# Kernel optimization log

Measured on AMD Instinct MI355X. Metric: run time of the kernel, lower is better.

## Reference

```python
import jax, jax.numpy as jnp
import numpy as np

B_, S_, D_ = 2, 1024, 768
EXPAND, HEADDIM, DSTATE = 2, 64, 64
DINNER = EXPAND * D_            # 1536
NHEADS = DINNER // HEADDIM      # 24
DMLP = int(2.5 * D_)            # 1920
PROJ = 2 * DINNER + 2 * NHEADS * DSTATE + NHEADS + NHEADS * (DSTATE // 2)  # 6936


def rms_norm(x, w, eps=1e-5):
    return x * jax.lax.rsqrt(jnp.mean(x * x, axis=-1, keepdims=True) + eps) * w


def apply_rope(x, angles):
    # x: (..., d_state), angles: (..., d_state//2)
    x1 = x[..., 0::2]
    x2 = x[..., 1::2]
    c, s = jnp.cos(angles), jnp.sin(angles)
    even = c * x1 - s * x2
    odd = s * x1 + c * x2
    return jnp.stack([even, odd], axis=-1).reshape(x.shape)


def ssm_scan(x, A, Bm, Cm):
    # x: (b,s,h,p), A: (b,s,h), Bm/Cm: (b,s,h,n)
    b, s, h, p = x.shape
    n = Bm.shape[-1]

    def step(hstate, inp):
        x_t, A_t, B_t, C_t = inp
        hstate = hstate * jnp.exp(A_t)[:, :, None, None] + jnp.einsum('bhn,bhp->bhpn', B_t, x_t)
        y_t = jnp.einsum('bhpn,bhn->bhp', hstate, C_t)
        return hstate, y_t

    h0 = jnp.zeros((b, h, p, n), dtype=x.dtype)
    xs = (jnp.swapaxes(x, 0, 1), jnp.swapaxes(A, 0, 1),
          jnp.swapaxes(Bm, 0, 1), jnp.swapaxes(Cm, 0, 1))
    _, ys = jax.lax.scan(step, h0, xs)
    return jnp.swapaxes(ys, 0, 1)  # (b,s,h,p)


def setup_inputs() -> dict:
    key = jax.random.key(0)
    ks = jax.random.split(key, 16)
    sc = 0.02
    return {
        'x': jax.random.normal(ks[0], (B_, S_, D_), dtype=jnp.float32),
        'norm1_w': jnp.ones((D_,), jnp.float32),
        'norm2_w': jnp.ones((D_,), jnp.float32),
        'in_proj_w': jax.random.normal(ks[1], (PROJ, D_), jnp.float32) * sc,
        'out_proj_w': jax.random.normal(ks[2], (D_, DINNER), jnp.float32) * sc,
        'A_log': jax.random.uniform(ks[3], (NHEADS,), jnp.float32, -4.0, -1.0),
        'D': jnp.ones((NHEADS,), jnp.float32),
        'dt_bias': jax.random.uniform(ks[4], (NHEADS,), jnp.float32, 0.001, 0.1),
        'B_bias': jnp.ones((1, NHEADS, DSTATE), jnp.float32),
        'C_bias': jnp.ones((1, NHEADS, DSTATE), jnp.float32),
        'Bnorm_w': jnp.ones((DSTATE,), jnp.float32),
        'Cnorm_w': jnp.ones((DSTATE,), jnp.float32),
        'mlp_gate_w': jax.random.normal(ks[5], (DMLP, D_), jnp.float32) * sc,
        'mlp_up_w': jax.random.normal(ks[6], (DMLP, D_), jnp.float32) * sc,
        'mlp_down_w': jax.random.normal(ks[7], (D_, DMLP), jnp.float32) * sc,
    }


def reference(x, norm1_w, norm2_w, in_proj_w, out_proj_w, A_log, D, dt_bias,
              B_bias, C_bias, Bnorm_w, Cnorm_w, mlp_gate_w, mlp_up_w, mlp_down_w):
    b, s, _ = x.shape
    h = rms_norm(x, norm1_w)
    proj = jnp.einsum('bsd,od->bso', h, in_proj_w)
    i = 0
    z = proj[..., i:i + DINNER]; i += DINNER
    x_ssm = proj[..., i:i + DINNER]; i += DINNER
    Bm = proj[..., i:i + NHEADS * DSTATE].reshape(b, s, NHEADS, DSTATE); i += NHEADS * DSTATE
    Cm = proj[..., i:i + NHEADS * DSTATE].reshape(b, s, NHEADS, DSTATE); i += NHEADS * DSTATE
    dt = proj[..., i:i + NHEADS]; i += NHEADS
    theta = proj[..., i:].reshape(b, s, NHEADS, DSTATE // 2)

    dt = jax.nn.softplus(dt + dt_bias)                 # (b,s,h)
    A = -jnp.exp(A_log) * dt                           # (b,s,h)
    alpha = jnp.exp(A)
    gamma = (alpha - 1.0) / (A + 1e-6) * 0.5 + 1.0

    Bm = rms_norm(Bm, Bnorm_w) + B_bias
    Cm = rms_norm(Cm, Cnorm_w) + C_bias
    cum_theta = jnp.cumsum(dt[..., None] * theta, axis=1)
    Bm = apply_rope(Bm, cum_theta)
    Cm = apply_rope(Cm, cum_theta)

    x_ssm = x_ssm.reshape(b, s, NHEADS, HEADDIM)
    x_scaled = x_ssm * gamma[..., None]
    y = ssm_scan(x_scaled, A, Bm, Cm)                  # (b,s,h,p)
    skip = (D[None, None, :] * x_ssm.sum(-1))[..., None]  # (b,s,h,1)
    y = (y + skip).reshape(b, s, DINNER)
    y = y * (z * jax.nn.sigmoid(z))
    y = jnp.einsum('bsi,oi->bso', y, out_proj_w)
    x = x + y
    h2 = rms_norm(x, norm2_w)
    g = jnp.einsum('bsd,od->bso', h2, mlp_gate_w)
    u = jnp.einsum('bsd,od->bso', h2, mlp_up_w)
    mlp = jnp.einsum('bsi,oi->bso', (g * jax.nn.sigmoid(g)) * u, mlp_down_w)
    return x + mlp
```

## Files before the change

kernel.cpp:

```cpp
#include <hip/hip_runtime.h>

typedef unsigned short u16;
typedef __attribute__((ext_vector_type(8))) short short8;
typedef __attribute__((ext_vector_type(4))) float f32x4;

constexpr int B_N    = 2;
constexpr int SEQ    = 1024;
constexpr int DMODEL = 768;
constexpr int DINNER = 1536;
constexpr int NH     = 24;
constexpr int DMLP   = 1920;
constexpr int NPROJ  = 6936;
constexpr int PP     = 7040;
constexpr int MROWS  = B_N * SEQ;
constexpr int NCHUNK = 16;
constexpr int CLEN   = 64;

__device__ __forceinline__ u16 f2bf(float f) {
  union { float f; unsigned u; } x; x.f = f;
  unsigned r = x.u + 0x7fffu + ((x.u >> 16) & 1u);
  return (u16)(r >> 16);
}
__device__ __forceinline__ float bf2f(u16 b) {
  union { unsigned u; float f; } x; x.u = ((unsigned)b) << 16; return x.f;
}

__device__ __forceinline__ void gld_lds16(const u16* g, u16* l) {
  __builtin_amdgcn_global_load_lds((const __attribute__((address_space(1))) void*)g,
                                   (__attribute__((address_space(3))) void*)l, 16, 0, 0);
}

__device__ __forceinline__ short8 frag(const u16* base, int row, int cb) {
  return *(const short8*)(base + row * 64 + ((cb ^ (row & 7)) << 3));
}
__device__ __forceinline__ int swz_idx(int row, int e) {
  return (((e >> 3) ^ (row & 7)) << 3) | (e & 7);
}

constexpr size_t E0  = (size_t)PP * DMODEL;
constexpr size_t E0s = (size_t)NPROJ * DMODEL;
constexpr size_t E1  = (size_t)DMODEL * DINNER;
constexpr size_t E2  = (size_t)DMLP * DMODEL;
constexpr size_t ETOT = E0 + E1 + 3 * E2;

__global__ void cast_all_kernel(const float* __restrict__ w_in, const float* __restrict__ w_out,
                                const float* __restrict__ w_g, const float* __restrict__ w_u,
                                const float* __restrict__ w_d,
                                u16* __restrict__ wb_in, u16* __restrict__ wb_out,
                                u16* __restrict__ wb_gu, u16* __restrict__ wb_d) {
  size_t i = ((size_t)blockIdx.x * 256 + threadIdx.x) * 4;
  if (i >= ETOT) return;
  float4 v; u16* dst;
  if (i < E0) {
    dst = wb_in + i;
    if (i < E0s) v = *(const float4*)(w_in + i);
    else { v.x = v.y = v.z = v.w = 0.f; }
  } else if (i < E0 + E1) {
    size_t k = i - E0; dst = wb_out + k; v = *(const float4*)(w_out + k);
  } else if (i < E0 + E1 + 2 * E2) {
    size_t k = i - E0 - E1;
    size_t r = k / DMODEL, col = k - r * DMODEL;
    const float* src = (r & 1) ? w_u : w_g;
    v = *(const float4*)(src + (r >> 1) * DMODEL + col);
    dst = wb_gu + k;
  } else {
    size_t k = i - E0 - E1 - 2 * E2; dst = wb_d + k; v = *(const float4*)(w_d + k);
  }
  short4 o;
  o.x = (short)f2bf(v.x); o.y = (short)f2bf(v.y);
  o.z = (short)f2bf(v.z); o.w = (short)f2bf(v.w);
  *(short4*)dst = o;
}

__global__ __launch_bounds__(256) void add_rmsnorm_kernel(
    const float* __restrict__ a, const float* __restrict__ b,
    const float* __restrict__ w, float* __restrict__ sum_out,
    u16* __restrict__ hout) {
  int row = blockIdx.x;
  int t = threadIdx.x;
  const float* pa = a + (size_t)row * DMODEL;
  const float* pb = b ? b + (size_t)row * DMODEL : nullptr;
  float v[3]; float ss = 0.f;
#pragma unroll
  for (int i = 0; i < 3; ++i) {
    int c = t + i * 256;
    float x = pa[c];
    if (pb) x += pb[c];
    v[i] = x; ss += x * x;
  }
#pragma unroll
  for (int o = 32; o > 0; o >>= 1) ss += __shfl_xor(ss, o);
  __shared__ float red[4];
  if ((t & 63) == 0) red[t >> 6] = ss;
  __syncthreads();
  ss = red[0] + red[1] + red[2] + red[3];
  float sc = rsqrtf(ss * (1.f / DMODEL) + 1e-5f);
#pragma unroll
  for (int i = 0; i < 3; ++i) {
    int c = t + i * 256;
    if (sum_out) sum_out[(size_t)row * DMODEL + c] = v[i];
    hout[(size_t)row * DMODEL + c] = f2bf(v[i] * sc * w[c]);
  }
}

template<int BM, int BN, int MODE>
__global__ __launch_bounds__(256) void gemm_bt_kernel(
    const u16* __restrict__ A, const u16* __restrict__ Bw,
    void* __restrict__ Cv, int K, int ldc, const float* __restrict__ addsrc) {
  constexpr int MI = BM / 32;
  constexpr int NJ = BN / 32;
  __shared__ u16 As[BM * 64];
  __shared__ u16 Bs[BN * 64];
  const int t = threadIdx.x;
  const int lane = t & 63;
  const int wave = t >> 6;
  const int wm = wave >> 1, wn = wave & 1;
  const int gx = gridDim.x, gy = gridDim.y;
  const int o = blockIdx.y * gx + blockIdx.x;
  const int nwg = gx * gy;
  const int cid = (o & 7) * (nwg >> 3) + (o >> 3);
  const int bx = cid / gy, by = cid - bx * gy;
  const int m0 = by * BM, n0 = bx * BN;
  f32x4 acc[MI][NJ] = {};
  const int rr = t >> 3;
  const int kc = (((t & 7) ^ (rr & 7))) * 8;
  const u16* ga = A + (size_t)(m0 + rr) * K + kc;
  const u16* gb = Bw + (size_t)(n0 + rr) * K + kc;
  for (int kt = 0; kt < K; kt += 64) {
    __syncthreads();
#pragma unroll
    for (int i = 0; i < MI; ++i)
      gld_lds16(ga + (size_t)i * 32 * K + kt, As + i * 2048 + t * 8);
#pragma unroll
    for (int i = 0; i < NJ; ++i)
      gld_lds16(gb + (size_t)i * 32 * K + kt, Bs + i * 2048 + t * 8);
    __syncthreads();
#pragma unroll
    for (int kh = 0; kh < 2; ++kh) {
      const int cq = kh * 4 + (lane >> 4);
      short8 af[MI], bfr[NJ];
#pragma unroll
      for (int i = 0; i < MI; ++i)
        af[i] = frag(As, wm * (BM / 2) + i * 16 + (lane & 15), cq);
#pragma unroll
      for (int j = 0; j < NJ; ++j)
        bfr[j] = frag(Bs, wn * (BN / 2) + j * 16 + (lane & 15), cq);
#pragma unroll
      for (int i = 0; i < MI; ++i)
#pragma unroll
        for (int j = 0; j < NJ; ++j)
          acc[i][j] = __builtin_amdgcn_mfma_f32_16x16x32_bf16(af[i], bfr[j], acc[i][j], 0, 0, 0);
    }
  }
  const int cr = (lane >> 4) * 4;
  const int cc = lane & 15;
#pragma unroll
  for (int i = 0; i < MI; ++i) {
#pragma unroll
    for (int j = 0; j < NJ; ++j) {
      int row = m0 + wm * (BM / 2) + i * 16 + cr;
      int col = n0 + wn * (BN / 2) + j * 16 + cc;
      if (MODE == 0) {
        float* C = (float*)Cv;
        float* cp = C + (size_t)row * ldc + col;
        if (addsrc) {
          const float* ap = addsrc + (size_t)row * ldc + col;
#pragma unroll
          for (int r = 0; r < 4; ++r) cp[(size_t)r * ldc] = acc[i][j][r] + ap[(size_t)r * ldc];
        } else {
#pragma unroll
          for (int r = 0; r < 4; ++r) cp[(size_t)r * ldc] = acc[i][j][r];
        }
      } else if (MODE == 1) {
        u16* C = (u16*)Cv;
#pragma unroll
        for (int r = 0; r < 4; ++r)
          C[(size_t)(row + r) * ldc + col] = f2bf(acc[i][j][r]);
      } else {
        u16* C = (u16*)Cv;
#pragma unroll
        for (int r = 0; r < 4; ++r) {
          float v = acc[i][j][r];
          float p = __shfl_xor(v, 1);
          if ((lane & 1) == 0) {
            float g = v, u = p;
            float res = g / (1.f + __expf(-g)) * u;
            C[(size_t)(row + r) * ldc + (col >> 1)] = f2bf(res);
          }
        }
      }
    }
  }
}

__global__ __launch_bounds__(256) void prep_kernel(
    u16* __restrict__ proj, const float* __restrict__ A_log,
    const float* __restrict__ Dv, const float* __restrict__ dt_bias,
    const float* __restrict__ B_bias, const float* __restrict__ C_bias,
    const float* __restrict__ Bnw, const float* __restrict__ Cnw,
    float* __restrict__ Abuf, float* __restrict__ skip_b,
    float* __restrict__ dtheta) {
  int wid = blockIdx.x * 4 + (threadIdx.x >> 6);
  int lane = threadIdx.x & 63;
  int m = wid / NH, h = wid - m * NH;
  u16* row = proj + (size_t)m * PP;

  float Braw = bf2f(row[3072 + h * 64 + lane]);
  float Craw = bf2f(row[4608 + h * 64 + lane]);
  float sb = Braw * Braw, sc2 = Craw * Craw;
#pragma unroll
  for (int o = 32; o > 0; o >>= 1) { sb += __shfl_xor(sb, o); sc2 += __shfl_xor(sc2, o); }
  float rb = rsqrtf(sb * (1.f / 64.f) + 1e-5f);
  float rc = rsqrtf(sc2 * (1.f / 64.f) + 1e-5f);
  row[3072 + h * 64 + lane] = f2bf(Braw * rb * Bnw[lane] + B_bias[h * 64 + lane]);
  row[4608 + h * 64 + lane] = f2bf(Craw * rc * Cnw[lane] + C_bias[h * 64 + lane]);

  float dtr = bf2f(row[6144 + h]) + dt_bias[h];
  float dt = dtr > 20.f ? dtr : log1pf(__expf(dtr));
  float A = -__expf(A_log[h]) * dt;
  float alpha = __expf(A);
  float gamma = (alpha - 1.f) / (A + 1e-6f) * 0.5f + 1.f;

  float xv = bf2f(row[1536 + h * 64 + lane]);
  float sx = xv;
#pragma unroll
  for (int o = 32; o > 0; o >>= 1) sx += __shfl_xor(sx, o);
  row[1536 + h * 64 + lane] = f2bf(xv * gamma);

  if (lane == 0) {
    Abuf[(size_t)m * NH + h] = A;
    skip_b[(size_t)m * NH + h] = Dv[h] * sx;
  }
  if (lane < 32) {
    float th = bf2f(row[6168 + h * 32 + lane]);
    dtheta[(size_t)m * 768 + h * 32 + lane] = dt * th;
  }
}

__global__ __launch_bounds__(256) void cumsum_a_kernel(float* __restrict__ dtheta,
                                                       float* __restrict__ ctot) {
  int bid = blockIdx.x;
  int cb = bid % 3, rest = bid / 3;
  int c = rest & 15, b = rest >> 4;
  int col = cb * 256 + threadIdx.x;
  float* p = dtheta + ((size_t)(b * SEQ + c * CLEN)) * 768 + col;
  float acc = 0.f;
#pragma unroll 4
  for (int s = 0; s < CLEN; ++s) {
    acc += p[(size_t)s * 768];
    p[(size_t)s * 768] = acc;
  }
  ctot[((size_t)b * NCHUNK + c) * 768 + col] = acc;
}

__global__ void cumsum_b_kernel(float* __restrict__ ctot) {
  int tid = blockIdx.x * 256 + threadIdx.x;
  int b = tid / 768, col = tid - b * 768;
  float pre = 0.f;
#pragma unroll
  for (int c = 0; c < NCHUNK; ++c) {
    size_t o = ((size_t)b * NCHUNK + c) * 768 + col;
    float v = ctot[o];
    ctot[o] = pre;
    pre += v;
  }
}

__global__ __launch_bounds__(256) void rope_kernel(
    u16* __restrict__ proj, const float* __restrict__ dtheta,
    const float* __restrict__ ctot) {
  int wid = blockIdx.x * 4 + (threadIdx.x >> 6);
  int lane = threadIdx.x & 63;
  int m = wid / NH, h = wid - m * NH;
  int j = lane & 31;
  int b = m >> 10;
  int c = (m >> 6) & 15;
  float ang = dtheta[(size_t)m * 768 + h * 32 + j] +
              ctot[((size_t)b * NCHUNK + c) * 768 + h * 32 + j];
  float sn, cs;
  __sincosf(ang, &sn, &cs);
  int base = (lane < 32) ? 3072 : 4608;
  unsigned* p = (unsigned*)(proj + (size_t)m * PP + base + h * 64) + j;
  unsigned v = *p;
  float x1 = bf2f((u16)(v & 0xffffu));
  float x2 = bf2f((u16)(v >> 16));
  *p = (unsigned)f2bf(cs * x1 - sn * x2) | ((unsigned)f2bf(sn * x1 + cs * x2) << 16);
}

__global__ __launch_bounds__(256) void scanA_kernel(
    const u16* __restrict__ proj, const float* __restrict__ Abuf,
    float* __restrict__ Lbuf, float* __restrict__ Hbuf,
    float* __restrict__ y1b) {
  int c = blockIdx.x & 15, bh = blockIdx.x >> 4;
  int b = bh / NH, h = bh - b * NH;
  int t = threadIdx.x, w = t >> 6, l = t & 63;
  __shared__ float sTmp[64][65];
  __shared__ u16 sBT[64 * 64];
  __shared__ u16 sXT[64 * 64];
  __shared__ u16 sGm[64 * 64];
  __shared__ float sRatio[64], sL[64];
  int m0 = b * SEQ + c * CLEN;
  if (w == 0) {
    float v = Abuf[(size_t)(m0 + l) * NH + h];
#pragma unroll
    for (int o = 1; o < 64; o <<= 1) {
      float u = __shfl_up(v, o);
      if (l >= o) v += u;
    }
    Lbuf[(size_t)(m0 + l) * NH + h] = v;
    sL[l] = v;
    float L63 = __shfl(v, 63);
    sRatio[l] = __expf(L63 - v);
  }
  int rr = t >> 2, q = t & 3;
  {
    const u16* row = proj + (size_t)(m0 + rr) * PP + 3072 + h * 64;
#pragma unroll
    for (int k = 0; k < 4; ++k) {
      int e = q * 16 + k * 4;
      short4 sv = *(const short4*)(row + e);
      float4 ov;
      ov.x = bf2f((u16)sv.x); ov.y = bf2f((u16)sv.y);
      ov.z = bf2f((u16)sv.z); ov.w = bf2f((u16)sv.w);
      *(float4*)&sTmp[rr][e] = ov;
    }
  }
  const u16* baseC = proj + (size_t)m0 * PP + 4608 + h * 64;
  const u16* baseB = proj + (size_t)m0 * PP + 3072 + h * 64;
  short8 cf[2], bgf[2][4];
#pragma unroll
  for (int kh = 0; kh < 2; ++kh) {
    int cq = kh * 4 + (l >> 4);
    cf[kh] = *(const short8*)(baseC + (size_t)(w * 16 + (l & 15)) * PP + cq * 8);
#pragma unroll
    for (int j = 0; j < 4; ++j)
      bgf[kh][j] = *(const short8*)(baseB + (size_t)(j * 16 + (l & 15)) * PP + cq * 8);
  }
  __syncthreads();
  f32x4 g4[4] = {};
#pragma unroll
  for (int kh = 0; kh < 2; ++kh)
#pragma unroll
    for (int j = 0; j < 4; ++j)
      g4[j] = __builtin_amdgcn_mfma_f32_16x16x32_bf16(cf[kh], bgf[kh][j], g4[j], 0, 0, 0);
  {
#pragma unroll
    for (int k = 0; k < 8; ++k) {
      int tw = (l + w * 8 + k) & 31;
      int t0 = tw * 2;
      float v0 = sTmp[t0][l] * sRatio[t0];
      float v1 = sTmp[t0 + 1][l] * sRatio[t0 + 1];
      unsigned pk = (unsigned)f2bf(v0) | ((unsigned)f2bf(v1) << 16);
      *(unsigned*)(sBT + l * 64 + swz_idx(l, t0)) = pk;
    }
  }
  __syncthreads();
  {
    const u16* row = proj + (size_t)(m0 + rr) * PP + 1536 + h * 64;
#pragma unroll
    for (int k = 0; k < 4; ++k) {
      int e = q * 16 + k * 4;
      short4 sv = *(const short4*)(row + e);
      float4 ov;
      ov.x = bf2f((u16)sv.x); ov.y = bf2f((u16)sv.y);
      ov.z = bf2f((u16)sv.z); ov.w = bf2f((u16)sv.w);
      *(float4*)&sTmp[rr][e] = ov;
    }
  }
  __syncthreads();
  {
#pragma unroll
    for (int k = 0; k < 8; ++k) {
      int tw = (l + w * 8 + k) & 31;
      int t0 = tw * 2;
      unsigned pk = (unsigned)f2bf(sTmp[t0][l]) | ((unsigned)f2bf(sTmp[t0 + 1][l]) << 16);
      *(unsigned*)(sXT + l * 64 + swz_idx(l, t0)) = pk;
    }
  }
  {
    int sr = w * 16 + ((l >> 4) << 2);
#pragma unroll
    for (int j = 0; j < 4; ++j) {
      int tc = j * 16 + (l & 15);
#pragma unroll
      for (int r = 0; r < 4; ++r) {
        int s = sr + r;
        float gv = (tc <= s) ? g4[j][r] * __expf(sL[s] - sL[tc]) : 0.f;
        sGm[s * 64 + swz_idx(s, tc)] = f2bf(gv);
      }
    }
  }
  __syncthreads();
  f32x4 y1[4] = {}, ho[4] = {};
#pragma unroll
  for (int kh = 0; kh < 2; ++kh) {
    int cq = kh * 4 + (l >> 4);
    short8 agm = frag(sGm, w * 16 + (l & 15), cq);
    short8 axt = frag(sXT, w * 16 + (l & 15), cq);
#pragma unroll
    for (int j = 0; j < 4; ++j) {
      y1[j] = __builtin_amdgcn_mfma_f32_16x16x32_bf16(agm, frag(sXT, j * 16 + (l & 15), cq), y1[j], 0, 0, 0);
      ho[j] = __builtin_amdgcn_mfma_f32_16x16x32_bf16(axt, frag(sBT, j * 16 + (l & 15), cq), ho[j], 0, 0, 0);
    }
  }
  float* Hp = Hbuf + ((size_t)(bh * NCHUNK + c)) * 4096;
  int pr = w * 16 + ((l >> 4) << 2);
#pragma unroll
  for (int j = 0; j < 4; ++j)
#pragma unroll
    for (int r = 0; r < 4; ++r)
      Hp[(size_t)(pr + r) * 64 + j * 16 + (l & 15)] = ho[j][r];
#pragma unroll
  for (int r = 0; r < 4; ++r) {
    int s = pr + r;
#pragma unroll
    for (int j = 0; j < 4; ++j)
      y1b[(size_t)(m0 + s) * DINNER + h * 64 + j * 16 + (l & 15)] = y1[j][r];
  }
}

__global__ __launch_bounds__(256) void scan2_kernel(
    float* __restrict__ Hbuf, const float* __restrict__ Lbuf) {
  int bh = blockIdx.x >> 4;
  int e = (blockIdx.x & 15) * 256 + threadIdx.x;
  int b = bh / NH, h = bh - b * NH;
  float S = 0.f;
  for (int c = 0; c < NCHUNK; ++c) {
    float* Hp = Hbuf + ((size_t)(bh * NCHUNK + c)) * 4096 + e;
    float P = __expf(Lbuf[(size_t)(b * SEQ + c * CLEN + CLEN - 1) * NH + h]);
    float v = *Hp;
    *Hp = S;
    S = P * S + v;
  }
}

__global__ __launch_bounds__(256) void scanB_kernel(
    const u16* __restrict__ proj, const float* __restrict__ Hbuf,
    const float* __restrict__ Lbuf, const float* __restrict__ skip_b,
    const float* __restrict__ y1b, u16* __restrict__ actb) {
  int c = blockIdx.x & 15, bh = blockIdx.x >> 4;
  int b = bh / NH, h = bh - b * NH;
  int t = threadIdx.x, w = t >> 6, l = t & 63;
  __shared__ float sL[64], sSkip[64];
  int m0 = b * SEQ + c * CLEN;
  if (w == 0) {
    sL[l] = Lbuf[(size_t)(m0 + l) * NH + h];
    sSkip[l] = skip_b[(size_t)(m0 + l) * NH + h];
  }
  const u16* baseC = proj + (size_t)m0 * PP + 4608 + h * 64;
  const float* Hp = Hbuf + ((size_t)(bh * NCHUNK + c)) * 4096;
  short8 cf[2], hf[2][4];
#pragma unroll
  for (int kh = 0; kh < 2; ++kh) {
    int cq = kh * 4 + (l >> 4);
    cf[kh] = *(const short8*)(baseC + (size_t)(w * 16 + (l & 15)) * PP + cq * 8);
#pragma unroll
    for (int j = 0; j < 4; ++j) {
      const float* hp = Hp + (size_t)(j * 16 + (l & 15)) * 64 + cq * 8;
      float4 a = *(const float4*)hp;
      float4 b2 = *(const float4*)(hp + 4);
      short8 hv;
      hv[0] = (short)f2bf(a.x);  hv[1] = (short)f2bf(a.y);
      hv[2] = (short)f2bf(a.z);  hv[3] = (short)f2bf(a.w);
      hv[4] = (short)f2bf(b2.x); hv[5] = (short)f2bf(b2.y);
      hv[6] = (short)f2bf(b2.z); hv[7] = (short)f2bf(b2.w);
      hf[kh][j] = hv;
    }
  }
  __syncthreads();
  f32x4 y2[4] = {};
#pragma unroll
  for (int kh = 0; kh < 2; ++kh)
#pragma unroll
    for (int j = 0; j < 4; ++j)
      y2[j] = __builtin_amdgcn_mfma_f32_16x16x32_bf16(cf[kh], hf[kh][j], y2[j], 0, 0, 0);
  int sr = w * 16 + ((l >> 4) << 2);
#pragma unroll
  for (int r = 0; r < 4; ++r) {
    int s = sr + r;
    float scale = __expf(sL[s]);
    float skp = sSkip[s];
    size_t mrow = (size_t)(m0 + s);
#pragma unroll
    for (int j = 0; j < 4; ++j) {
      int p = j * 16 + (l & 15);
      float y = y1b[mrow * DINNER + h * 64 + p] + scale * y2[j][r] + skp;
      float z = bf2f(proj[mrow * PP + h * 64 + p]);
      float sg = 1.f / (1.f + __expf(-z));
      actb[mrow * DINNER + h * 64 + p] = f2bf(y * z * sg);
    }
  }
}

extern "C" void kernel_launch(void* const* d_in, const int* in_sizes, int n_in,
                              void* d_out, int out_size, void* d_ws, size_t ws_size,
                              hipStream_t stream) {
  (void)in_sizes; (void)n_in; (void)out_size; (void)ws_size;
  const float* x      = (const float*)d_in[0];
  const float* n1w    = (const float*)d_in[1];
  const float* n2w    = (const float*)d_in[2];
  const float* w_in   = (const float*)d_in[3];
  const float* w_out  = (const float*)d_in[4];
  const float* A_log  = (const float*)d_in[5];
  const float* Dv     = (const float*)d_in[6];
  const float* dt_b   = (const float*)d_in[7];
  const float* B_bias = (const float*)d_in[8];
  const float* C_bias = (const float*)d_in[9];
  const float* Bnw    = (const float*)d_in[10];
  const float* Cnw    = (const float*)d_in[11];
  const float* w_g    = (const float*)d_in[12];
  const float* w_u    = (const float*)d_in[13];
  const float* w_d    = (const float*)d_in[14];
  float* out = (float*)d_out;

  char* ws = (char*)d_ws;
  size_t off = 0;
  auto alloc = [&](size_t bytes) -> char* {
    char* p = ws + off;
    off = (off + bytes + 255) & ~(size_t)255;
    return p;
  };
  u16*   wb_in  = (u16*)  alloc(E0 * 2);
  u16*   wb_out = (u16*)  alloc(E1 * 2);
  u16*   wb_gu  = (u16*)  alloc(E2 * 2 * 2);
  u16*   wb_d   = (u16*)  alloc(E2 * 2);
  u16*   h1     = (u16*)  alloc((size_t)MROWS * DMODEL * 2);
  u16*   proj   = (u16*)  alloc((size_t)MROWS * PP * 2);
  float* Abuf   = (float*)alloc((size_t)MROWS * NH * 4);
  float* skip_b = (float*)alloc((size_t)MROWS * NH * 4);
  float* Lbuf   = (float*)alloc((size_t)MROWS * NH * 4);
  float* dtheta = (float*)alloc((size_t)MROWS * 768 * 4);
  float* ctot   = (float*)alloc((size_t)B_N * NCHUNK * 768 * 4);
  float* Hbuf   = (float*)alloc((size_t)B_N * NH * NCHUNK * 4096 * 4);
  float* y1b    = (float*)alloc((size_t)MROWS * DINNER * 4);
  u16*   actb   = (u16*)  alloc((size_t)MROWS * DINNER * 2);
  float* tmp1   = (float*)alloc((size_t)MROWS * DMODEL * 4);
  float* x2     = (float*)alloc((size_t)MROWS * DMODEL * 4);
  u16*   h2     = (u16*)  alloc((size_t)MROWS * DMODEL * 2);
  u16*   gub    = (u16*)  alloc((size_t)MROWS * DMLP * 2);

  cast_all_kernel<<<(int)((ETOT / 4 + 255) / 256), 256, 0, stream>>>(
      w_in, w_out, w_g, w_u, w_d, wb_in, wb_out, wb_gu, wb_d);
  add_rmsnorm_kernel<<<MROWS, 256, 0, stream>>>(x, nullptr, n1w, nullptr, h1);
  {
    dim3 g(PP / 128, MROWS / 64);
    gemm_bt_kernel<64, 128, 1><<<g, 256, 0, stream>>>(h1, wb_in, proj, DMODEL, PP, nullptr);
  }
  prep_kernel<<<MROWS * NH / 4, 256, 0, stream>>>(proj, A_log, Dv, dt_b, B_bias, C_bias,
                                                  Bnw, Cnw, Abuf, skip_b, dtheta);
  cumsum_a_kernel<<<B_N * NCHUNK * 3, 256, 0, stream>>>(dtheta, ctot);
  cumsum_b_kernel<<<6, 256, 0, stream>>>(ctot);
  rope_kernel<<<MROWS * NH / 4, 256, 0, stream>>>(proj, dtheta, ctot);
  scanA_kernel<<<B_N * NH * NCHUNK, 256, 0, stream>>>(proj, Abuf, Lbuf, Hbuf, y1b);
  scan2_kernel<<<B_N * NH * NCHUNK, 256, 0, stream>>>(Hbuf, Lbuf);
  scanB_kernel<<<B_N * NH * NCHUNK, 256, 0, stream>>>(proj, Hbuf, Lbuf, skip_b, y1b, actb);
  {
    dim3 g(DMODEL / 64, MROWS / 64);
    gemm_bt_kernel<64, 64, 0><<<g, 256, 0, stream>>>(actb, wb_out, tmp1, DINNER, DMODEL, nullptr);
  }
  add_rmsnorm_kernel<<<MROWS, 256, 0, stream>>>(x, tmp1, n2w, x2, h2);
  {
    dim3 g(2 * DMLP / 128, MROWS / 64);
    gemm_bt_kernel<64, 128, 2><<<g, 256, 0, stream>>>(h2, wb_gu, gub, DMODEL, DMLP, nullptr);
  }
  {
    dim3 g(DMODEL / 64, MROWS / 64);
    gemm_bt_kernel<64, 64, 0><<<g, 256, 0, stream>>>(gub, wb_d, out, DMLP, DMODEL, x2);
  }
}
```

Baseline: 283.0 us.

## Double-buffer GEMM LDS tiles and fuse weight cast with first RMSNorm

The GEMM kernel now keeps two LDS buffers and prefetches the next K-tile while computing on the current one, needing one barrier per iteration instead of two. The weight cast kernel and the first RMSNorm are merged into a single launch, with extra blocks doing the norm rows. This aims to hide global-to-LDS latency and save one launch. In exchange the GEMM uses twice the LDS, which may reduce occupancy.

```diff
diff --git a/kernel.cpp b/kernel.cpp
--- a/kernel.cpp
+++ b/kernel.cpp
@@ -42,12 +42,48 @@
 constexpr size_t E1  = (size_t)DMODEL * DINNER;
 constexpr size_t E2  = (size_t)DMLP * DMODEL;
 constexpr size_t ETOT = E0 + E1 + 3 * E2;
-
-__global__ void cast_all_kernel(const float* __restrict__ w_in, const float* __restrict__ w_out,
-                                const float* __restrict__ w_g, const float* __restrict__ w_u,
-                                const float* __restrict__ w_d,
-                                u16* __restrict__ wb_in, u16* __restrict__ wb_out,
-                                u16* __restrict__ wb_gu, u16* __restrict__ wb_d) {
+constexpr int NCASTBLK = (int)((ETOT / 4 + 255) / 256);
+
+__device__ __forceinline__ void rmsnorm_body(
+    int row, int t, const float* __restrict__ a, const float* __restrict__ b,
+    const float* __restrict__ w, float* __restrict__ sum_out, u16* __restrict__ hout) {
+  const float* pa = a + (size_t)row * DMODEL;
+  const float* pb = b ? b + (size_t)row * DMODEL : nullptr;
+  float v[3]; float ss = 0.f;
+#pragma unroll
+  for (int i = 0; i < 3; ++i) {
+    int c = t + i * 256;
+    float x = pa[c];
+    if (pb) x += pb[c];
+    v[i] = x; ss += x * x;
+  }
+#pragma unroll
+  for (int o = 32; o > 0; o >>= 1) ss += __shfl_xor(ss, o);
+  __shared__ float red[4];
+  if ((t & 63) == 0) red[t >> 6] = ss;
+  __syncthreads();
+  ss = red[0] + red[1] + red[2] + red[3];
+  float sc = rsqrtf(ss * (1.f / DMODEL) + 1e-5f);
+#pragma unroll
+  for (int i = 0; i < 3; ++i) {
+    int c = t + i * 256;
+    if (sum_out) sum_out[(size_t)row * DMODEL + c] = v[i];
+    hout[(size_t)row * DMODEL + c] = f2bf(v[i] * sc * w[c]);
+  }
+}
+
+__global__ __launch_bounds__(256) void cast_norm_kernel(
+    const float* __restrict__ w_in, const float* __restrict__ w_out,
+    const float* __restrict__ w_g, const float* __restrict__ w_u,
+    const float* __restrict__ w_d,
+    u16* __restrict__ wb_in, u16* __restrict__ wb_out,
+    u16* __restrict__ wb_gu, u16* __restrict__ wb_d,
+    const float* __restrict__ x, const float* __restrict__ n1w,
+    u16* __restrict__ h1) {
+  if (blockIdx.x >= NCASTBLK) {
+    rmsnorm_body(blockIdx.x - NCASTBLK, threadIdx.x, x, nullptr, n1w, nullptr, h1);
+    return;
+  }
   size_t i = ((size_t)blockIdx.x * 256 + threadIdx.x) * 4;
   if (i >= ETOT) return;
   float4 v; u16* dst;
@@ -76,31 +112,7 @@
     const float* __restrict__ a, const float* __restrict__ b,
     const float* __restrict__ w, float* __restrict__ sum_out,
     u16* __restrict__ hout) {
-  int row = blockIdx.x;
-  int t = threadIdx.x;
-  const float* pa = a + (size_t)row * DMODEL;
-  const float* pb = b ? b + (size_t)row * DMODEL : nullptr;
-  float v[3]; float ss = 0.f;
-#pragma unroll
-  for (int i = 0; i < 3; ++i) {
-    int c = t + i * 256;
-    float x = pa[c];
-    if (pb) x += pb[c];
-    v[i] = x; ss += x * x;
-  }
-#pragma unroll
-  for (int o = 32; o > 0; o >>= 1) ss += __shfl_xor(ss, o);
-  __shared__ float red[4];
-  if ((t & 63) == 0) red[t >> 6] = ss;
-  __syncthreads();
-  ss = red[0] + red[1] + red[2] + red[3];
-  float sc = rsqrtf(ss * (1.f / DMODEL) + 1e-5f);
-#pragma unroll
-  for (int i = 0; i < 3; ++i) {
-    int c = t + i * 256;
-    if (sum_out) sum_out[(size_t)row * DMODEL + c] = v[i];
-    hout[(size_t)row * DMODEL + c] = f2bf(v[i] * sc * w[c]);
-  }
+  rmsnorm_body(blockIdx.x, threadIdx.x, a, b, w, sum_out, hout);
 }
 
 template<int BM, int BN, int MODE>
@@ -109,8 +121,10 @@
     void* __restrict__ Cv, int K, int ldc, const float* __restrict__ addsrc) {
   constexpr int MI = BM / 32;
   constexpr int NJ = BN / 32;
-  __shared__ u16 As[BM * 64];
-  __shared__ u16 Bs[BN * 64];
+  constexpr int ASZ = BM * 64;
+  constexpr int BSZ = BN * 64;
+  __shared__ u16 As[2 * ASZ];
+  __shared__ u16 Bs[2 * BSZ];
   const int t = threadIdx.x;
   const int lane = t & 63;
   const int wave = t >> 6;
@@ -126,31 +140,44 @@
   const int kc = (((t & 7) ^ (rr & 7))) * 8;
   const u16* ga = A + (size_t)(m0 + rr) * K + kc;
   const u16* gb = Bw + (size_t)(n0 + rr) * K + kc;
+#pragma unroll
+  for (int i = 0; i < MI; ++i)
+    gld_lds16(ga + (size_t)i * 32 * K, As + i * 2048 + t * 8);
+#pragma unroll
+  for (int i = 0; i < NJ; ++i)
+    gld_lds16(gb + (size_t)i * 32 * K, Bs + i * 2048 + t * 8);
+  __syncthreads();
+  int cur = 0;
   for (int kt = 0; kt < K; kt += 64) {
-    __syncthreads();
-#pragma unroll
-    for (int i = 0; i < MI; ++i)
-      gld_lds16(ga + (size_t)i * 32 * K + kt, As + i * 2048 + t * 8);
-#pragma unroll
-    for (int i = 0; i < NJ; ++i)
-      gld_lds16(gb + (size_t)i * 32 * K + kt, Bs + i * 2048 + t * 8);
-    __syncthreads();
+    const int nxt = cur ^ 1;
+    if (kt + 64 < K) {
+#pragma unroll
+      for (int i = 0; i < MI; ++i)
+        gld_lds16(ga + (size_t)i * 32 * K + kt + 64, As + nxt * ASZ + i * 2048 + t * 8);
+#pragma unroll
+      for (int i = 0; i < NJ; ++i)
+        gld_lds16(gb + (size_t)i * 32 * K + kt + 64, Bs + nxt * BSZ + i * 2048 + t * 8);
+    }
+    const u16* ab = As + cur * ASZ;
+    const u16* bb = Bs + cur * BSZ;
 #pragma unroll
     for (int kh = 0; kh < 2; ++kh) {
       const int cq = kh * 4 + (lane >> 4);
       short8 af[MI], bfr[NJ];
 #pragma unroll
       for (int i = 0; i < MI; ++i)
-        af[i] = frag(As, wm * (BM / 2) + i * 16 + (lane & 15), cq);
+        af[i] = frag(ab, wm * (BM / 2) + i * 16 + (lane & 15), cq);
 #pragma unroll
       for (int j = 0; j < NJ; ++j)
-        bfr[j] = frag(Bs, wn * (BN / 2) + j * 16 + (lane & 15), cq);
+        bfr[j] = frag(bb, wn * (BN / 2) + j * 16 + (lane & 15), cq);
 #pragma unroll
       for (int i = 0; i < MI; ++i)
 #pragma unroll
         for (int j = 0; j < NJ; ++j)
           acc[i][j] = __builtin_amdgcn_mfma_f32_16x16x32_bf16(af[i], bfr[j], acc[i][j], 0, 0, 0);
     }
+    __syncthreads();
+    cur = nxt;
   }
   const int cr = (lane >> 4) * 4;
   const int cc = lane & 15;
@@ -539,9 +566,8 @@
   u16*   h2     = (u16*)  alloc((size_t)MROWS * DMODEL * 2);
   u16*   gub    = (u16*)  alloc((size_t)MROWS * DMLP * 2);
 
-  cast_all_kernel<<<(int)((ETOT / 4 + 255) / 256), 256, 0, stream>>>(
-      w_in, w_out, w_g, w_u, w_d, wb_in, wb_out, wb_gu, wb_d);
-  add_rmsnorm_kernel<<<MROWS, 256, 0, stream>>>(x, nullptr, n1w, nullptr, h1);
+  cast_norm_kernel<<<NCASTBLK + MROWS, 256, 0, stream>>>(
+      w_in, w_out, w_g, w_u, w_d, wb_in, wb_out, wb_gu, wb_d, x, n1w, h1);
   {
     dim3 g(PP / 128, MROWS / 64);
     gemm_bt_kernel<64, 128, 1><<<g, 256, 0, stream>>>(h1, wb_in, proj, DMODEL, PP, nullptr);
```

Result: slower. 294.4 us (+4.0%).
